# Kernel optimization log

Hardware: AMD Instinct MI355X
Metric: run time of the kernel (lower is better)

## Reference

```python
import jax, jax.numpy as jnp
import numpy as np

B1, B2, N, D = 1, 128, 256, 256
H, C = 8, 32
OUT = 256


def setup_inputs() -> dict:
    key = jax.random.key(0)
    ks = jax.random.split(key, 8)
    in_data = jax.random.normal(ks[0], (B1, B2, N, D), dtype=jnp.float32)
    # binary mask, mostly unmasked
    mask = (jax.random.uniform(ks[1], (B1, B2, N)) > 0.1).astype(jnp.float32)
    nonbatched_bias = jax.random.normal(ks[2], (B1, H, N, N), dtype=jnp.float32)
    scale = 1.0 / np.sqrt(D)
    w_qkv = jax.random.normal(ks[3], (3 * H * C, D), dtype=jnp.float32) * scale  # torch Linear [out,in]
    w_gate = jax.random.normal(ks[4], (H * C, D), dtype=jnp.float32) * scale
    gating_bias = jnp.ones((H * C,), dtype=jnp.float32)
    w_o = jax.random.normal(ks[5], (OUT, H * C), dtype=jnp.float32) * scale
    b_o = jnp.zeros((OUT,), dtype=jnp.float32)
    return {
        "in_data": in_data,
        "mask": mask,
        "nonbatched_bias": nonbatched_bias,
        "w_qkv": w_qkv,
        "w_gate": w_gate,
        "gating_bias": gating_bias,
        "w_o": w_o,
        "b_o": b_o,
    }


def reference(in_data, mask, nonbatched_bias, w_qkv, w_gate, gating_bias, w_o, b_o):
    scaling = C ** (-0.5)
    # fused QKV projection (no bias): [b1,b2,n, 3*h*c]
    qkv = jnp.einsum("xynd,ed->xyne", in_data, w_qkv)
    q, k, v = jnp.split(qkv, 3, axis=-1)

    def heads(t):  # [b1,b2,n,h*c] -> [b1,b2,h,n,c]
        return t.reshape(B1, B2, N, H, C).transpose(0, 1, 3, 2, 4)

    q, k, v = heads(q) * scaling, heads(k), heads(v)
    logits = jnp.einsum("xyhqc,xyhkc->xyhqk", q, k)
    mask_bias = (1e9 * (mask - 1.0))[:, :, None, None, :]  # [b1,b2,1,1,n]
    logits = logits + mask_bias + nonbatched_bias[:, None]  # [b1,b2,h,q,k]
    weights = jax.nn.softmax(logits, axis=-1)
    wa = jnp.einsum("xyhqk,xyhkc->xyhqc", weights, v)
    wa = wa.transpose(0, 1, 3, 2, 4).reshape(B1, B2, N, H * C)
    # sigmoid gating: sigmoid(gate_linear(x) + gating_bias) * weighted_avg
    gate = jax.nn.sigmoid(jnp.einsum("xynd,ed->xyne", in_data, w_gate) + gating_bias)
    wa = gate * wa
    out = jnp.einsum("xyne,oe->xyno", wa, w_o) + b_o
    return out
```

## Files before the change

kernel.cpp:

```cpp
#include <hip/hip_runtime.h>
#include <stdint.h>

#define B2 128
#define NSEQ 256
#define DIM 256
#define NH 8
#define CH 32

typedef __attribute__((ext_vector_type(8))) __bf16 bf16x8;
typedef __attribute__((ext_vector_type(8))) unsigned short u16x8;
typedef __attribute__((ext_vector_type(4))) unsigned short u16x4;
typedef __attribute__((ext_vector_type(4))) float f32x4;

__device__ __forceinline__ unsigned short f2bf(float f) {
  unsigned int u = __builtin_bit_cast(unsigned int, f);
  u += 0x7FFFu + ((u >> 16) & 1u);
  return (unsigned short)(u >> 16);
}
__device__ __forceinline__ float bf2f(unsigned short h) {
  unsigned int u = ((unsigned int)h) << 16;
  return __builtin_bit_cast(float, u);
}
__device__ __forceinline__ bf16x8 as_bf(u16x8 v) { return __builtin_bit_cast(bf16x8, v); }

__device__ __forceinline__ void gload16(void* lds, const void* g) {
  __builtin_amdgcn_global_load_lds(
      (__attribute__((address_space(1))) void*)(g),
      (__attribute__((address_space(3))) void*)(lds), 16, 0, 0);
}

__global__ void k_convert(const float* __restrict__ x, const float* __restrict__ wqkv,
                          const float* __restrict__ wgate, const float* __restrict__ wo,
                          unsigned short* __restrict__ xb, unsigned short* __restrict__ wallb,
                          unsigned short* __restrict__ wob) {
  const int NX = 8388608, NWALL = 262144, NWO = 65536;
  int i = blockIdx.x * blockDim.x + threadIdx.x;
  int total4 = (NX + NWALL + NWO) >> 2;
  if (i >= total4) return;
  int e = i << 2;
  float4 v;
  unsigned short* dst;
  if (e < NX) {
    v = *reinterpret_cast<const float4*>(x + e);
    dst = xb + e;
  } else if (e < NX + NWALL) {
    int o = e - NX;
    v = (o < 196608) ? *reinterpret_cast<const float4*>(wqkv + o)
                     : *reinterpret_cast<const float4*>(wgate + (o - 196608));
    dst = wallb + o;
  } else {
    int o = e - NX - NWALL;
    v = *reinterpret_cast<const float4*>(wo + o);
    dst = wob + o;
  }
  u16x4 r;
  r[0] = f2bf(v.x); r[1] = f2bf(v.y); r[2] = f2bf(v.z); r[3] = f2bf(v.w);
  *reinterpret_cast<u16x4*>(dst) = r;
}

template <int MODE>
__launch_bounds__(256, 2)
__global__ void k_gemm(const unsigned short* __restrict__ A, const unsigned short* __restrict__ Bw,
                       unsigned short* __restrict__ qs, unsigned short* __restrict__ ksb,
                       unsigned short* __restrict__ vsb, unsigned short* __restrict__ gateb,
                       const float* __restrict__ gbias,
                       float* __restrict__ outp, const float* __restrict__ bo) {
  __shared__ __attribute__((aligned(16))) unsigned short As[2][8192];
  __shared__ __attribute__((aligned(16))) unsigned short Bs[2][8192];
  const int tid = threadIdx.x, lane = tid & 63, w = tid >> 6;
  const int wr = w >> 1, wc = w & 1;
  const int m0 = blockIdx.x * 128, n0 = blockIdx.y * 128;

  auto stage = [&](unsigned short* sbuf, const unsigned short* gsrc, int row0, int k0) {
#pragma unroll
    for (int q2 = 0; q2 < 4; ++q2) {
      int ob = (w * 4 + q2) * 1024 + (lane << 4);
      int r = ob >> 7, cb = ob & 127;
      int scb = cb ^ ((r & 7) << 4);
      const unsigned short* g = gsrc + (size_t)(row0 + r) * 256 + k0 + (scb >> 1);
      gload16(sbuf + (size_t)(w * 4 + q2) * 512, g);
    }
  };

  f32x4 acc[4][4];
#pragma unroll
  for (int i = 0; i < 4; ++i) {
#pragma unroll
    for (int j = 0; j < 4; ++j) acc[i][j] = (f32x4){0.f, 0.f, 0.f, 0.f};
  }

  stage(As[0], A, m0, 0);
  stage(Bs[0], Bw, n0, 0);
  asm volatile("s_waitcnt vmcnt(0)" ::: "memory");
  __syncthreads();

#pragma unroll
  for (int kt = 0; kt < 4; ++kt) {
    const int cur = kt & 1;
    if (kt < 3) {
      stage(As[cur ^ 1], A, m0, (kt + 1) * 64);
      stage(Bs[cur ^ 1], Bw, n0, (kt + 1) * 64);
    }
#pragma unroll
    for (int kk = 0; kk < 2; ++kk) {
      bf16x8 af[4], bfv[4];
      const int cb = kk * 64 + ((lane >> 4) << 4);
#pragma unroll
      for (int fr = 0; fr < 4; ++fr) {
        int ra = wr * 64 + fr * 16 + (lane & 15);
        int off = ra * 128 + (cb ^ ((ra & 7) << 4));
        af[fr] = *reinterpret_cast<const bf16x8*>((const char*)As[cur] + off);
      }
#pragma unroll
      for (int fc = 0; fc < 4; ++fc) {
        int rb = wc * 64 + fc * 16 + (lane & 15);
        int off = rb * 128 + (cb ^ ((rb & 7) << 4));
        bfv[fc] = *reinterpret_cast<const bf16x8*>((const char*)Bs[cur] + off);
      }
#pragma unroll
      for (int fr = 0; fr < 4; ++fr) {
#pragma unroll
        for (int fc = 0; fc < 4; ++fc)
          acc[fr][fc] = __builtin_amdgcn_mfma_f32_16x16x32_bf16(af[fr], bfv[fc], acc[fr][fc], 0, 0, 0);
      }
    }
    asm volatile("s_waitcnt vmcnt(0)" ::: "memory");
    __syncthreads();
  }

  if (MODE == 0) {
#pragma unroll
    for (int fr = 0; fr < 4; ++fr) {
      int mrow = m0 + wr * 64 + fr * 16 + ((lane >> 4) << 2);
      int b = mrow >> 8, n = mrow & 255;
#pragma unroll
      for (int fc = 0; fc < 4; ++fc) {
        int e = n0 + wc * 64 + fc * 16 + (lane & 15);
        int which = e >> 8, loc = e & 255, hh = loc >> 5, cc = loc & 31;
#pragma unroll
        for (int i = 0; i < 4; ++i) {
          float v = acc[fr][fc][i];
          size_t idx = ((size_t)(b * 8 + hh) * 256 + (n + i)) * 32 + cc;
          if (which == 0) {
            qs[idx] = f2bf(v * 0.17677669529663687f);
          } else if (which == 1) {
            ksb[idx] = f2bf(v);
          } else if (which == 2) {
            vsb[idx] = f2bf(v);
          } else {
            float gsig = 1.0f / (1.0f + __expf(-(v + gbias[loc])));
            gateb[idx] = f2bf(gsig);
          }
        }
      }
    }
  } else {
#pragma unroll
    for (int fr = 0; fr < 4; ++fr) {
      int mrow = m0 + wr * 64 + fr * 16 + ((lane >> 4) << 2);
#pragma unroll
      for (int fc = 0; fc < 4; ++fc) {
        int e = n0 + wc * 64 + fc * 16 + (lane & 15);
        float bb = bo[e];
#pragma unroll
        for (int i = 0; i < 4; ++i)
          outp[(size_t)(mrow + i) * 256 + e] = acc[fr][fc][i] + bb;
      }
    }
  }
}

__launch_bounds__(256, 3)
__global__ void k_attn(const unsigned short* __restrict__ qs, const unsigned short* __restrict__ ksb,
                       const unsigned short* __restrict__ vsb, const unsigned short* __restrict__ gateb,
                       const float* __restrict__ mask, const float* __restrict__ nb,
                       unsigned short* __restrict__ wag) {
  __shared__ __attribute__((aligned(16))) unsigned short vt[32][264];
  __shared__ __attribute__((aligned(16))) unsigned short pch[4][2][16][72];
  __shared__ __attribute__((aligned(16))) float mb[256];
  __shared__ float invl[4][16];
  const int tid = threadIdx.x, lane = tid & 63, w = tid >> 6;
  const int l15 = lane & 15, hi = lane >> 4;
  const int b = blockIdx.x, h = blockIdx.y;
  const size_t bh = (size_t)(b * 8 + h);
  const unsigned short* kbase = ksb + bh * 8192;
  const unsigned short* vbase = vsb + bh * 8192;
  const unsigned short* qbase = qs + bh * 8192;
  const float* nbh = nb + (size_t)h * 65536;

  mb[tid] = 1e9f * (mask[b * 256 + tid] - 1.0f);
  {
    const unsigned short* vrow = vbase + tid * 32;
#pragma unroll
    for (int c0 = 0; c0 < 32; c0 += 8) {
      u16x8 vv = *reinterpret_cast<const u16x8*>(vrow + c0);
#pragma unroll
      for (int j = 0; j < 8; ++j) vt[c0 + j][tid] = vv[j];
    }
  }
  u16x8 kf[16];
#pragma unroll
  for (int kt = 0; kt < 16; ++kt)
    kf[kt] = *reinterpret_cast<const u16x8*>(kbase + (kt * 16 + l15) * 32 + hi * 8);
  __syncthreads();

  const f32x4 zero = {0.f, 0.f, 0.f, 0.f};
#pragma unroll 1
  for (int fr = 0; fr < 4; ++fr) {
    const int q0 = w * 64 + fr * 16;
    u16x8 qf = *reinterpret_cast<const u16x8*>(qbase + (q0 + l15) * 32 + hi * 8);
    f32x4 sacc[16];
    __builtin_amdgcn_s_setprio(1);
#pragma unroll
    for (int kt = 0; kt < 16; ++kt)
      sacc[kt] = __builtin_amdgcn_mfma_f32_16x16x32_bf16(as_bf(kf[kt]), as_bf(qf), zero, 0, 0, 0);
    __builtin_amdgcn_s_setprio(0);

    const float* nbq = nbh + (size_t)(q0 + l15) * 256;
#pragma unroll
    for (int kt = 0; kt < 16; ++kt) {
      float4 nb4 = *reinterpret_cast<const float4*>(nbq + kt * 16 + hi * 4);
      float4 mb4 = *reinterpret_cast<const float4*>(&mb[kt * 16 + hi * 4]);
      sacc[kt][0] += mb4.x + nb4.x;
      sacc[kt][1] += mb4.y + nb4.y;
      sacc[kt][2] += mb4.z + nb4.z;
      sacc[kt][3] += mb4.w + nb4.w;
    }
    float mx = -3.0e38f;
#pragma unroll
    for (int kt = 0; kt < 16; ++kt) {
#pragma unroll
      for (int i = 0; i < 4; ++i) mx = fmaxf(mx, sacc[kt][i]);
    }
    mx = fmaxf(mx, __shfl_xor(mx, 16));
    mx = fmaxf(mx, __shfl_xor(mx, 32));

    float sum = 0.f;
    f32x4 wacc[2];
    wacc[0] = zero; wacc[1] = zero;
#pragma unroll
    for (int c = 0; c < 4; ++c) {
      const int buf = c & 1;
#pragma unroll
      for (int ktl = 0; ktl < 4; ++ktl) {
        const int kt = c * 4 + ktl;
        u16x4 pv;
#pragma unroll
        for (int i = 0; i < 4; ++i) {
          float p = __expf(sacc[kt][i] - mx);
          sum += p;
          pv[i] = f2bf(p);
        }
        *reinterpret_cast<u16x4*>(&pch[w][buf][l15][ktl * 16 + hi * 4]) = pv;
      }
      asm volatile("s_waitcnt lgkmcnt(0)" ::: "memory");
      __builtin_amdgcn_sched_barrier(0);
      __builtin_amdgcn_s_setprio(1);
#pragma unroll
      for (int ks2 = 0; ks2 < 2; ++ks2) {
        bf16x8 pa = *reinterpret_cast<const bf16x8*>(&pch[w][buf][l15][ks2 * 32 + hi * 8]);
#pragma unroll
        for (int ct = 0; ct < 2; ++ct) {
          bf16x8 vb = *reinterpret_cast<const bf16x8*>(&vt[ct * 16 + l15][c * 64 + ks2 * 32 + hi * 8]);
          wacc[ct] = __builtin_amdgcn_mfma_f32_16x16x32_bf16(pa, vb, wacc[ct], 0, 0, 0);
        }
      }
      __builtin_amdgcn_s_setprio(0);
    }
    sum += __shfl_xor(sum, 16);
    sum += __shfl_xor(sum, 32);
    const float inv = 1.0f / sum;
    if (hi == 0) invl[w][l15] = inv;

    float* et = reinterpret_cast<float*>(&pch[w][0][0][0]);
#pragma unroll
    for (int ct = 0; ct < 2; ++ct) {
#pragma unroll
      for (int i = 0; i < 4; ++i)
        et[(hi * 4 + i) * 36 + ct * 16 + l15] = wacc[ct][i];
    }
    asm volatile("s_waitcnt lgkmcnt(0)" ::: "memory");
    __builtin_amdgcn_sched_barrier(0);
    const int eq = lane >> 2, eh = lane & 3;
    float4 v0 = *reinterpret_cast<const float4*>(&et[eq * 36 + eh * 8]);
    float4 v1 = *reinterpret_cast<const float4*>(&et[eq * 36 + eh * 8 + 4]);
    const float iv = invl[w][eq];
    const int qrow = q0 + eq;
    u16x8 g = *reinterpret_cast<const u16x8*>(gateb + bh * 8192 + qrow * 32 + eh * 8);
    u16x8 ov;
    ov[0] = f2bf(bf2f(g[0]) * v0.x * iv);
    ov[1] = f2bf(bf2f(g[1]) * v0.y * iv);
    ov[2] = f2bf(bf2f(g[2]) * v0.z * iv);
    ov[3] = f2bf(bf2f(g[3]) * v0.w * iv);
    ov[4] = f2bf(bf2f(g[4]) * v1.x * iv);
    ov[5] = f2bf(bf2f(g[5]) * v1.y * iv);
    ov[6] = f2bf(bf2f(g[6]) * v1.z * iv);
    ov[7] = f2bf(bf2f(g[7]) * v1.w * iv);
    *reinterpret_cast<u16x8*>(wag + ((size_t)(b * 256 + qrow)) * 256 + h * 32 + eh * 8) = ov;
    asm volatile("s_waitcnt lgkmcnt(0)" ::: "memory");
    __builtin_amdgcn_sched_barrier(0);
  }
}

extern "C" void kernel_launch(void* const* d_in, const int* in_sizes, int n_in,
                              void* d_out, int out_size, void* d_ws, size_t ws_size,
                              hipStream_t stream) {
  const float* x     = (const float*)d_in[0];
  const float* mask  = (const float*)d_in[1];
  const float* nb    = (const float*)d_in[2];
  const float* wqkv  = (const float*)d_in[3];
  const float* wgate = (const float*)d_in[4];
  const float* gbias = (const float*)d_in[5];
  const float* wo    = (const float*)d_in[6];
  const float* bo    = (const float*)d_in[7];
  float* outp = (float*)d_out;

  char* ws = (char*)d_ws;
  unsigned short* xb    = (unsigned short*)(ws);
  unsigned short* wallb = (unsigned short*)(ws + 16777216);
  unsigned short* wob   = (unsigned short*)(ws + 17301504);
  unsigned short* qs    = (unsigned short*)(ws + 17432576);
  unsigned short* ksb   = (unsigned short*)(ws + 34209792);
  unsigned short* vsb   = (unsigned short*)(ws + 50987008);
  unsigned short* gateb = (unsigned short*)(ws + 67764224);
  unsigned short* wag   = xb;

  k_convert<<<dim3(8512), dim3(256), 0, stream>>>(x, wqkv, wgate, wo, xb, wallb, wob);
  k_gemm<0><<<dim3(256, 8), dim3(256), 0, stream>>>(xb, wallb, qs, ksb, vsb, gateb, gbias, nullptr, nullptr);
  k_attn<<<dim3(128, 8), dim3(256), 0, stream>>>(qs, ksb, vsb, gateb, mask, nb, wag);
  k_gemm<1><<<dim3(256, 2), dim3(256), 0, stream>>>(wag, wob, nullptr, nullptr, nullptr, nullptr, nullptr, outp, bo);
}
```

Measured before the change: 139.7 us.

## Halve GEMM K-tile to shrink LDS and raise occupancy; pin K fragments in registers

The projection GEMM's K-step drops from 64 to 32, with 8 double-buffered iterations instead of 4. This halves shared memory per block, and launch bounds are raised to 4 blocks per CU for higher occupancy. The swizzle and address math are adjusted for the 64-byte rows. In the attention kernel, an empty asm constraint forces each K fragment to be materialized in VGPRs up front. The cost is twice as many barriers and waits per GEMM tile, and a possibly tighter register budget under the new launch bound.

Result: no change. 142.0 us (+1.6%).

```diff
diff --git a/kernel.cpp b/kernel.cpp
--- a/kernel.cpp
+++ b/kernel.cpp
@@ -59,26 +59,27 @@
 }
 
 template <int MODE>
-__launch_bounds__(256, 2)
+__launch_bounds__(256, 4)
 __global__ void k_gemm(const unsigned short* __restrict__ A, const unsigned short* __restrict__ Bw,
                        unsigned short* __restrict__ qs, unsigned short* __restrict__ ksb,
                        unsigned short* __restrict__ vsb, unsigned short* __restrict__ gateb,
                        const float* __restrict__ gbias,
                        float* __restrict__ outp, const float* __restrict__ bo) {
-  __shared__ __attribute__((aligned(16))) unsigned short As[2][8192];
-  __shared__ __attribute__((aligned(16))) unsigned short Bs[2][8192];
+  __shared__ __attribute__((aligned(16))) unsigned short As[2][4096];
+  __shared__ __attribute__((aligned(16))) unsigned short Bs[2][4096];
   const int tid = threadIdx.x, lane = tid & 63, w = tid >> 6;
   const int wr = w >> 1, wc = w & 1;
+  const int l15 = lane & 15, hi = lane >> 4;
   const int m0 = blockIdx.x * 128, n0 = blockIdx.y * 128;
 
   auto stage = [&](unsigned short* sbuf, const unsigned short* gsrc, int row0, int k0) {
 #pragma unroll
-    for (int q2 = 0; q2 < 4; ++q2) {
-      int ob = (w * 4 + q2) * 1024 + (lane << 4);
-      int r = ob >> 7, cb = ob & 127;
-      int scb = cb ^ ((r & 7) << 4);
+    for (int q2 = 0; q2 < 2; ++q2) {
+      int ob = (w * 2 + q2) * 1024 + (lane << 4);
+      int r = ob >> 6, cb = ob & 63;
+      int scb = cb ^ ((r & 3) << 4);
       const unsigned short* g = gsrc + (size_t)(row0 + r) * 256 + k0 + (scb >> 1);
-      gload16(sbuf + (size_t)(w * 4 + q2) * 512, g);
+      gload16(sbuf + (size_t)(w * 2 + q2) * 512, g);
     }
   };
 
@@ -95,26 +96,25 @@
   __syncthreads();
 
 #pragma unroll
-  for (int kt = 0; kt < 4; ++kt) {
+  for (int kt = 0; kt < 8; ++kt) {
     const int cur = kt & 1;
-    if (kt < 3) {
-      stage(As[cur ^ 1], A, m0, (kt + 1) * 64);
-      stage(Bs[cur ^ 1], Bw, n0, (kt + 1) * 64);
-    }
-#pragma unroll
-    for (int kk = 0; kk < 2; ++kk) {
+    if (kt < 7) {
+      stage(As[cur ^ 1], A, m0, (kt + 1) * 32);
+      stage(Bs[cur ^ 1], Bw, n0, (kt + 1) * 32);
+    }
+    {
       bf16x8 af[4], bfv[4];
-      const int cb = kk * 64 + ((lane >> 4) << 4);
+      const int cbx = hi << 4;
 #pragma unroll
       for (int fr = 0; fr < 4; ++fr) {
-        int ra = wr * 64 + fr * 16 + (lane & 15);
-        int off = ra * 128 + (cb ^ ((ra & 7) << 4));
+        int ra = wr * 64 + fr * 16 + l15;
+        int off = ra * 64 + (cbx ^ ((ra & 3) << 4));
         af[fr] = *reinterpret_cast<const bf16x8*>((const char*)As[cur] + off);
       }
 #pragma unroll
       for (int fc = 0; fc < 4; ++fc) {
-        int rb = wc * 64 + fc * 16 + (lane & 15);
-        int off = rb * 128 + (cb ^ ((rb & 7) << 4));
+        int rb = wc * 64 + fc * 16 + l15;
+        int off = rb * 64 + (cbx ^ ((rb & 3) << 4));
         bfv[fc] = *reinterpret_cast<const bf16x8*>((const char*)Bs[cur] + off);
       }
 #pragma unroll
@@ -131,11 +131,11 @@
   if (MODE == 0) {
 #pragma unroll
     for (int fr = 0; fr < 4; ++fr) {
-      int mrow = m0 + wr * 64 + fr * 16 + ((lane >> 4) << 2);
+      int mrow = m0 + wr * 64 + fr * 16 + (hi << 2);
       int b = mrow >> 8, n = mrow & 255;
 #pragma unroll
       for (int fc = 0; fc < 4; ++fc) {
-        int e = n0 + wc * 64 + fc * 16 + (lane & 15);
+        int e = n0 + wc * 64 + fc * 16 + l15;
         int which = e >> 8, loc = e & 255, hh = loc >> 5, cc = loc & 31;
 #pragma unroll
         for (int i = 0; i < 4; ++i) {
@@ -157,10 +157,10 @@
   } else {
 #pragma unroll
     for (int fr = 0; fr < 4; ++fr) {
-      int mrow = m0 + wr * 64 + fr * 16 + ((lane >> 4) << 2);
+      int mrow = m0 + wr * 64 + fr * 16 + (hi << 2);
 #pragma unroll
       for (int fc = 0; fc < 4; ++fc) {
-        int e = n0 + wc * 64 + fc * 16 + (lane & 15);
+        int e = n0 + wc * 64 + fc * 16 + l15;
         float bb = bo[e];
 #pragma unroll
         for (int i = 0; i < 4; ++i)
@@ -198,10 +198,12 @@
       for (int j = 0; j < 8; ++j) vt[c0 + j][tid] = vv[j];
     }
   }
-  u16x8 kf[16];
-#pragma unroll
-  for (int kt = 0; kt < 16; ++kt)
-    kf[kt] = *reinterpret_cast<const u16x8*>(kbase + (kt * 16 + l15) * 32 + hi * 8);
+  u16x8 kfu[16];
+#pragma unroll
+  for (int kt = 0; kt < 16; ++kt) {
+    kfu[kt] = *reinterpret_cast<const u16x8*>(kbase + (kt * 16 + l15) * 32 + hi * 8);
+    asm volatile("" : "+v"(kfu[kt]));
+  }
   __syncthreads();
 
   const f32x4 zero = {0.f, 0.f, 0.f, 0.f};
@@ -209,11 +211,12 @@
   for (int fr = 0; fr < 4; ++fr) {
     const int q0 = w * 64 + fr * 16;
     u16x8 qf = *reinterpret_cast<const u16x8*>(qbase + (q0 + l15) * 32 + hi * 8);
+
     f32x4 sacc[16];
     __builtin_amdgcn_s_setprio(1);
 #pragma unroll
     for (int kt = 0; kt < 16; ++kt)
-      sacc[kt] = __builtin_amdgcn_mfma_f32_16x16x32_bf16(as_bf(kf[kt]), as_bf(qf), zero, 0, 0, 0);
+      sacc[kt] = __builtin_amdgcn_mfma_f32_16x16x32_bf16(as_bf(kfu[kt]), as_bf(qf), zero, 0, 0, 0);
     __builtin_amdgcn_s_setprio(0);
 
     const float* nbq = nbh + (size_t)(q0 + l15) * 256;
```
